# Performance work log

Hardware: AMD Instinct MI355X
Metric: run time of the kernel (lower is better)

Reference implementation:

```python
import jax, jax.numpy as jnp
import numpy as np

N_NODES = 100000
N_EDGES = 1000000
D = 64
N_LAYERS = 3
N_GRAPHS = 64


def _sage_layer(x, src, dst, W_l, b_l, W_r, n_nodes):
    # PyG SAGEConv (aggr='mean'): out = lin_l(mean_{j in N(i)} x_j) + lin_r(x_i)
    msgs = x[src]  # [E, d] gather
    agg = jax.ops.segment_sum(msgs, dst, num_segments=n_nodes)  # [N, d]
    deg = jax.ops.segment_sum(jnp.ones((src.shape[0],), x.dtype), dst, num_segments=n_nodes)
    agg = agg / jnp.maximum(deg, 1.0)[:, None]
    return agg @ W_l + b_l + x @ W_r


def setup_inputs() -> dict:
    key = jax.random.key(0)
    k = jax.random.split(key, 6)
    scale = 1.0 / np.sqrt(D)
    x = jax.random.normal(k[0], (N_NODES, D), dtype=jnp.float32)
    edge_index = jax.random.randint(k[1], (2, N_EDGES), 0, N_NODES, dtype=jnp.int64)
    batch = jnp.sort(jax.random.randint(k[2], (N_NODES,), 0, N_GRAPHS, dtype=jnp.int64))
    Wl = jax.random.normal(k[3], (N_LAYERS, D, D), dtype=jnp.float32) * scale
    bl = jax.random.normal(k[4], (N_LAYERS, D), dtype=jnp.float32) * scale
    Wr = jax.random.normal(k[5], (N_LAYERS, D, D), dtype=jnp.float32) * scale
    return {"x": x, "edge_index": edge_index, "batch": batch,
            "Wl": Wl, "bl": bl, "Wr": Wr, "num_graphs": N_GRAPHS}


def reference(x, edge_index, batch, Wl, bl, Wr, num_graphs):
    src, dst = edge_index[0], edge_index[1]
    n_nodes = x.shape[0]
    for l in range(Wl.shape[0]):  # small fixed number of layers
        x = _sage_layer(x, src, dst, Wl[l], bl[l], Wr[l], n_nodes)
    # per-graph masked mean pooling == segment mean over batch ids
    sums = jax.ops.segment_sum(x, batch, num_segments=num_graphs)  # [G, d]
    counts = jax.ops.segment_sum(jnp.ones((n_nodes,), x.dtype), batch, num_segments=num_graphs)
    return sums / jnp.maximum(counts, 1.0)[:, None]
```

## Files before the change

### kernel.cpp

```cpp
#include <hip/hip_runtime.h>


#define DD 64
#define NBA 128
#define CAP 4096

typedef __attribute__((ext_vector_type(8))) short short8;
typedef __attribute__((ext_vector_type(4))) float f32x4;

__device__ inline short8 pack4(unsigned a, unsigned b, unsigned c, unsigned d) {
    union { uint4 u; short8 s; } un;
    un.u = make_uint4(a, b, c, d);
    return un.s;
}

__device__ inline short8 as_short8(uint4 u) {
    union { uint4 u4; short8 s; } un;
    un.u4 = u;
    return un.s;
}

__device__ inline unsigned rne_bf16(float v) {
    unsigned u = __float_as_uint(v);
    return (u + 0x7FFFu + ((u >> 16) & 1u)) >> 16;
}

__global__ __launch_bounds__(256) void bucket_count(
    const int* __restrict__ dst, int* __restrict__ cnt, int E, int NBUCK) {
    extern __shared__ int hist[];
    const int b = blockIdx.x;
    const int per = (E + NBA - 1) / NBA;
    const int lo = b * per, hi = min(lo + per, E);
    for (int k = threadIdx.x; k < NBUCK; k += 256) hist[k] = 0;
    __syncthreads();
    for (int e = lo + threadIdx.x; e < hi; e += 256)
        atomicAdd(&hist[dst[e] >> 8], 1);
    __syncthreads();
    for (int k = threadIdx.x; k < NBUCK; k += 256)
        cnt[b * NBUCK + k] = hist[k];
}

__global__ __launch_bounds__(256) void bucket_prescan(
    const int* __restrict__ cnt, int* __restrict__ base,
    int* __restrict__ tot, int NBUCK) {
    const int lane = threadIdx.x & 63;
    const int k = (int)((blockIdx.x * 256 + threadIdx.x) >> 6);
    if (k >= NBUCK) return;
    int v0 = cnt[(size_t)lane * NBUCK + k];
    int v1 = cnt[(size_t)(lane + 64) * NBUCK + k];
    int s0 = v0, s1 = v1;
#pragma unroll
    for (int o = 1; o < 64; o <<= 1) {
        const int u0 = __shfl_up(s0, o, 64);
        const int u1 = __shfl_up(s1, o, 64);
        if (lane >= o) { s0 += u0; s1 += u1; }
    }
    const int total0 = __shfl(s0, 63, 64);
    base[(size_t)lane * NBUCK + k] = s0 - v0;
    base[(size_t)(lane + 64) * NBUCK + k] = total0 + s1 - v1;
    if (lane == 63) tot[k] = total0 + s1;
}

__global__ __launch_bounds__(1024) void bucket_toff(
    const int* __restrict__ tot, int* __restrict__ boff,
    int* __restrict__ offs, int NBUCK, int E, int N) {
    __shared__ int s[1024];
    __shared__ int carry_s;
    const int t = threadIdx.x;
    if (t == 0) carry_s = 0;
    __syncthreads();
    for (int cs = 0; cs < NBUCK; cs += 1024) {
        const int i = cs + t;
        const int v = (i < NBUCK) ? tot[i] : 0;
        s[t] = v;
        __syncthreads();
        for (int o = 1; o < 1024; o <<= 1) {
            const int a = (t >= o) ? s[t - o] : 0;
            __syncthreads();
            s[t] += a;
            __syncthreads();
        }
        const int carry = carry_s;
        if (i < NBUCK) boff[i] = carry + s[t] - v;
        __syncthreads();
        if (t == 1023) carry_s = carry + s[1023];
        __syncthreads();
    }
    if (t == 0) { boff[NBUCK] = E; offs[N] = E; }
}

__global__ __launch_bounds__(256) void bucket_scatter(
    const int* __restrict__ src, const int* __restrict__ dst,
    const int* __restrict__ base, const int* __restrict__ boff,
    unsigned* __restrict__ ebuf, int E, int NBUCK) {
    extern __shared__ int pos[];
    const int b = blockIdx.x;
    const int per = (E + NBA - 1) / NBA;
    const int lo = b * per, hi = min(lo + per, E);
    for (int k = threadIdx.x; k < NBUCK; k += 256)
        pos[k] = base[b * NBUCK + k] + boff[k];
    __syncthreads();
    for (int e = lo + threadIdx.x; e < hi; e += 256) {
        const int d = dst[e];
        const int s = src[e];
        const int p = atomicAdd(&pos[d >> 8], 1);
        ebuf[p] = ((unsigned)(d & 255) << 24) | (unsigned)s;
    }
}

__global__ __launch_bounds__(256) void bucket_sort(
    const unsigned* __restrict__ ebuf, const int* __restrict__ boff,
    int* __restrict__ offs, int* __restrict__ adj, int N) {
    const int b  = blockIdx.x;
    const int lo = boff[b];
    const int sz = boff[b + 1] - lo;
    const int base = b << 8;
    const int t = threadIdx.x;

    __shared__ int hist[256];
    __shared__ int hcur[256];
    __shared__ unsigned sbuf[CAP];

    hist[t] = 0;
    __syncthreads();
    for (int i = t; i < sz; i += 256)
        atomicAdd(&hist[ebuf[lo + i] >> 24], 1);
    __syncthreads();
    int v = hist[t];
    hcur[t] = v;
    __syncthreads();
    for (int o = 1; o < 256; o <<= 1) {
        const int a = (t >= o) ? hcur[t - o] : 0;
        __syncthreads();
        hcur[t] += a;
        __syncthreads();
    }
    const int ex = hcur[t] - v;
    __syncthreads();
    hcur[t] = ex;
    if (base + t < N) offs[base + t] = lo + ex;
    __syncthreads();

    if (sz <= CAP) {
        for (int i = t; i < sz; i += 256) {
            const unsigned w = ebuf[lo + i];
            const int p = atomicAdd(&hcur[w >> 24], 1);
            sbuf[p] = w & 0x00FFFFFFu;
        }
        __syncthreads();
        for (int i = t; i < sz; i += 256) adj[lo + i] = (int)sbuf[i];
    } else {
        for (int i = t; i < sz; i += 256) {
            const unsigned w = ebuf[lo + i];
            const int p = atomicAdd(&hcur[w >> 24], 1);
            adj[lo + p] = (int)(w & 0x00FFFFFFu);
        }
    }
}

__global__ __launch_bounds__(256) void cast_bf16(
    const float* __restrict__ in, unsigned short* __restrict__ outb, long long n8) {
    const long long t = (long long)blockIdx.x * 256 + threadIdx.x;
    if (t >= n8) return;
    const float4 v0 = *reinterpret_cast<const float4*>(in + t * 8);
    const float4 v1 = *reinterpret_cast<const float4*>(in + t * 8 + 4);
    uint4 o;
    o.x = rne_bf16(v0.x) | (rne_bf16(v0.y) << 16);
    o.y = rne_bf16(v0.z) | (rne_bf16(v0.w) << 16);
    o.z = rne_bf16(v1.x) | (rne_bf16(v1.y) << 16);
    o.w = rne_bf16(v1.z) | (rne_bf16(v1.w) << 16);
    *reinterpret_cast<uint4*>(outb + t * 8) = o;
}

__global__ __launch_bounds__(256) void aggregate_bf16(
    const unsigned short* __restrict__ xb, float* __restrict__ agg,
    const int* __restrict__ offs, const int* __restrict__ adj, int n) {
    const int t  = blockIdx.x * 256 + threadIdx.x;
    const int nd = t >> 3;
    const int c8 = (t & 7) * 8;
    if (nd >= n) return;

    const int s = offs[nd];
    const int e = offs[nd + 1];

    float a0[8], a1[8], a2[8], a3[8];
#pragma unroll
    for (int p = 0; p < 8; ++p) { a0[p] = 0.f; a1[p] = 0.f; a2[p] = 0.f; a3[p] = 0.f; }

#define ACC8(A, U)                                                             \
    do {                                                                       \
        A[0] += __uint_as_float((U).x << 16);                                  \
        A[1] += __uint_as_float((U).x & 0xFFFF0000u);                          \
        A[2] += __uint_as_float((U).y << 16);                                  \
        A[3] += __uint_as_float((U).y & 0xFFFF0000u);                          \
        A[4] += __uint_as_float((U).z << 16);                                  \
        A[5] += __uint_as_float((U).z & 0xFFFF0000u);                          \
        A[6] += __uint_as_float((U).w << 16);                                  \
        A[7] += __uint_as_float((U).w & 0xFFFF0000u);                          \
    } while (0)

    int j = s;
    for (; j + 4 <= e; j += 4) {
        const int i0 = adj[j], i1 = adj[j + 1], i2 = adj[j + 2], i3 = adj[j + 3];
        const uint4 u0 = *reinterpret_cast<const uint4*>(xb + (size_t)i0 * DD + c8);
        const uint4 u1 = *reinterpret_cast<const uint4*>(xb + (size_t)i1 * DD + c8);
        const uint4 u2 = *reinterpret_cast<const uint4*>(xb + (size_t)i2 * DD + c8);
        const uint4 u3 = *reinterpret_cast<const uint4*>(xb + (size_t)i3 * DD + c8);
        ACC8(a0, u0); ACC8(a1, u1); ACC8(a2, u2); ACC8(a3, u3);
    }
    for (; j < e; ++j) {
        const uint4 u = *reinterpret_cast<const uint4*>(xb + (size_t)adj[j] * DD + c8);
        ACC8(a0, u);
    }
#undef ACC8

    const int deg = e - s;
    const float inv = (deg > 0) ? (1.0f / (float)deg) : 1.0f;
    float4 r0, r1;
    r0.x = (a0[0] + a1[0] + a2[0] + a3[0]) * inv;
    r0.y = (a0[1] + a1[1] + a2[1] + a3[1]) * inv;
    r0.z = (a0[2] + a1[2] + a2[2] + a3[2]) * inv;
    r0.w = (a0[3] + a1[3] + a2[3] + a3[3]) * inv;
    r1.x = (a0[4] + a1[4] + a2[4] + a3[4]) * inv;
    r1.y = (a0[5] + a1[5] + a2[5] + a3[5]) * inv;
    r1.z = (a0[6] + a1[6] + a2[6] + a3[6]) * inv;
    r1.w = (a0[7] + a1[7] + a2[7] + a3[7]) * inv;
    *reinterpret_cast<float4*>(agg + (size_t)nd * DD + c8)     = r0;
    *reinterpret_cast<float4*>(agg + (size_t)nd * DD + c8 + 4) = r1;
}

__global__ void pack_B(const float* __restrict__ Wl, const float* __restrict__ Wr,
                       unsigned* __restrict__ Bp, int L) {
    int t = blockIdx.x * 256 + threadIdx.x;
    int wv = t >> 6, lane = t & 63;
    if (wv >= L * 16) return;
    int layer = wv >> 4;
    int fid = wv & 15;
    int ks = fid >> 2, nt = fid & 3;
    int j = nt * 16 + (lane & 15);
    int kb = ks * 32 + (lane >> 4) * 8;
    const float* wl = Wl + (size_t)layer * DD * DD;
    const float* wr = Wr + (size_t)layer * DD * DD;
    unsigned hi[8], lo[8];
#pragma unroll
    for (int s = 0; s < 8; ++s) {
        int k = kb + s;
        float v = (k < DD) ? wl[k * DD + j] : wr[(k - DD) * DD + j];
        unsigned u = __float_as_uint(v);
        unsigned h = u & 0xFFFF0000u;
        hi[s] = h;
        float lf = v - __uint_as_float(h);
        lo[s] = __float_as_uint(lf) & 0xFFFF0000u;
    }
    size_t base_hi = ((size_t)(layer * 2 + 0) * 16 + fid) * 64 + lane;
    size_t base_lo = ((size_t)(layer * 2 + 1) * 16 + fid) * 64 + lane;
#pragma unroll
    for (int p = 0; p < 4; ++p) {
        Bp[base_hi * 4 + p] = (hi[2 * p] >> 16) | hi[2 * p + 1];
        Bp[base_lo * 4 + p] = (lo[2 * p] >> 16) | lo[2 * p + 1];
    }
}

__global__ __launch_bounds__(256, 2) void mfma_gemm(
    const float* __restrict__ g, const unsigned short* __restrict__ xb,
    unsigned short* __restrict__ outb, const unsigned* __restrict__ Bp,
    const float* __restrict__ bias, int n) {
    const int lane = threadIdx.x & 63;
    const int wv   = (int)((blockIdx.x * 256 + threadIdx.x) >> 6);
    const int nwv  = (int)((gridDim.x * 256) >> 6);

    short8 Bh[4][4], Bl[4][4];
#pragma unroll
    for (int ks = 0; ks < 4; ++ks)
#pragma unroll
        for (int nt = 0; nt < 4; ++nt) {
            int fid = ks * 4 + nt;
            const uint4 h = *reinterpret_cast<const uint4*>(Bp + ((size_t)fid * 64 + lane) * 4);
            const uint4 l = *reinterpret_cast<const uint4*>(Bp + ((size_t)(16 + fid) * 64 + lane) * 4);
            Bh[ks][nt] = pack4(h.x, h.y, h.z, h.w);
            Bl[ks][nt] = pack4(l.x, l.y, l.z, l.w);
        }

    float bv[4];
#pragma unroll
    for (int nt = 0; nt < 4; ++nt) bv[nt] = bias[nt * 16 + (lane & 15)];

    const int ntiles = (n + 15) >> 4;
    for (int tile = wv; tile < ntiles; tile += nwv) {
        const int row = tile * 16 + (lane & 15);
        const bool ok = row < n;
        const float*          grow = g  + (size_t)row * DD + (lane >> 4) * 8;
        const unsigned short* xrow = xb + (size_t)row * DD + (lane >> 4) * 8;

        f32x4 acc[4];
#pragma unroll
        for (int nt = 0; nt < 4; ++nt) acc[nt] = (f32x4){bv[nt], bv[nt], bv[nt], bv[nt]};

#pragma unroll
        for (int ks = 0; ks < 2; ++ks) {
            const float* base = grow + ks * 32;
            f32x4 v0 = ok ? *reinterpret_cast<const f32x4*>(base)
                          : (f32x4){0.f, 0.f, 0.f, 0.f};
            f32x4 v1 = ok ? *reinterpret_cast<const f32x4*>(base + 4)
                          : (f32x4){0.f, 0.f, 0.f, 0.f};
            float vv[8] = {v0[0], v0[1], v0[2], v0[3], v1[0], v1[1], v1[2], v1[3]};
            unsigned hu[4], lu[4];
#pragma unroll
            for (int p = 0; p < 4; ++p) {
                unsigned ua = __float_as_uint(vv[2 * p]);
                unsigned ub = __float_as_uint(vv[2 * p + 1]);
                unsigned ha = ua & 0xFFFF0000u, hb = ub & 0xFFFF0000u;
                hu[p] = (ha >> 16) | hb;
                float la = vv[2 * p]     - __uint_as_float(ha);
                float lb = vv[2 * p + 1] - __uint_as_float(hb);
                lu[p] = ((__float_as_uint(la) & 0xFFFF0000u) >> 16) |
                        (__float_as_uint(lb) & 0xFFFF0000u);
            }
            const short8 Ah = pack4(hu[0], hu[1], hu[2], hu[3]);
            const short8 Al = pack4(lu[0], lu[1], lu[2], lu[3]);
#pragma unroll
            for (int nt = 0; nt < 4; ++nt) {
                acc[nt] = __builtin_amdgcn_mfma_f32_16x16x32_bf16(Ah, Bh[ks][nt], acc[nt], 0, 0, 0);
                acc[nt] = __builtin_amdgcn_mfma_f32_16x16x32_bf16(Al, Bh[ks][nt], acc[nt], 0, 0, 0);
                acc[nt] = __builtin_amdgcn_mfma_f32_16x16x32_bf16(Ah, Bl[ks][nt], acc[nt], 0, 0, 0);
            }
        }

#pragma unroll
        for (int ks = 2; ks < 4; ++ks) {
            const uint4 u = ok ? *reinterpret_cast<const uint4*>(xrow + (ks & 1) * 32)
                               : make_uint4(0, 0, 0, 0);
            const short8 Ah = as_short8(u);
#pragma unroll
            for (int nt = 0; nt < 4; ++nt) {
                acc[nt] = __builtin_amdgcn_mfma_f32_16x16x32_bf16(Ah, Bh[ks][nt], acc[nt], 0, 0, 0);
                acc[nt] = __builtin_amdgcn_mfma_f32_16x16x32_bf16(Ah, Bl[ks][nt], acc[nt], 0, 0, 0);
            }
        }

        const int r0 = tile * 16 + (lane >> 4) * 4;
#pragma unroll
        for (int r = 0; r < 4; ++r) {
            const int rr = r0 + r;
            if (rr < n) {
#pragma unroll
                for (int nt = 0; nt < 4; ++nt) {
                    const size_t idx = (size_t)rr * DD + nt * 16 + (lane & 15);
                    outb[idx] = (unsigned short)rne_bf16(acc[nt][r]);
                }
            }
        }
    }
}

__global__ __launch_bounds__(256) void pool_partial2(
    const float* __restrict__ xa, const unsigned short* __restrict__ xb,
    const int* __restrict__ batch,
    float* __restrict__ sumsA, float* __restrict__ sumsB, int n) {
    const int lane = threadIdx.x & 63;
    const int wv   = (int)((blockIdx.x * blockDim.x + threadIdx.x) >> 6);
    const int nwv  = (int)((gridDim.x * blockDim.x) >> 6);
    const int chunk = (n + nwv - 1) / nwv;
    const int start = wv * chunk;
    if (start >= n) return;
    const int end = min(start + chunk, n);

    int g = batch[start];
    float accA = 0.f, accB = 0.f;
    for (int nd = start; nd < end; ++nd) {
        const int bg = batch[nd];
        if (bg != g) {
            atomicAdd(&sumsA[(size_t)g * DD + lane], accA);
            atomicAdd(&sumsB[(size_t)g * DD + lane], accB);
            accA = 0.f; accB = 0.f;
            g = bg;
        }
        accA += xa[(size_t)nd * DD + lane];
        accB += __uint_as_float((unsigned)xb[(size_t)nd * DD + lane] << 16);
    }
    atomicAdd(&sumsA[(size_t)g * DD + lane], accA);
    atomicAdd(&sumsB[(size_t)g * DD + lane], accB);
}

__global__ void final_gemm(const float* __restrict__ sumsA, const float* __restrict__ sumsX,
                           const int* __restrict__ batch,
                           const float* __restrict__ Wl, const float* __restrict__ bl,
                           const float* __restrict__ Wr,
                           float* __restrict__ out, int n) {
    const int g = blockIdx.x;
    const int d = threadIdx.x;

    int lo = 0, hi = n;
    while (lo < hi) { int m = (lo + hi) >> 1; if (batch[m] < g) lo = m + 1; else hi = m; }
    const int st = lo;
    lo = 0; hi = n;
    while (lo < hi) { int m = (lo + hi) >> 1; if (batch[m] < g + 1) lo = m + 1; else hi = m; }
    const int c = lo - st;

    if (c == 0) {
        out[(size_t)g * DD + d] = 0.f;
        return;
    }
    const float inv = 1.0f / (float)c;

    __shared__ float sa[DD], sx[DD];
    sa[d] = sumsA[(size_t)g * DD + d] * inv;
    sx[d] = sumsX[(size_t)g * DD + d] * inv;
    __syncthreads();

    float acc = bl[d];
#pragma unroll 8
    for (int k = 0; k < DD; ++k) acc += sa[k] * Wl[k * DD + d];
#pragma unroll 8
    for (int k = 0; k < DD; ++k) acc += sx[k] * Wr[k * DD + d];
    out[(size_t)g * DD + d] = acc;
}

extern "C" void kernel_launch(void* const* d_in, const int* in_sizes, int n_in,
                              void* d_out, int out_size, void* d_ws, size_t ws_size,
                              hipStream_t stream) {
    const float* x     = (const float*)d_in[0];
    const int*   ei    = (const int*)d_in[1];
    const int*   batch = (const int*)d_in[2];
    const float* Wl    = (const float*)d_in[3];
    const float* bl    = (const float*)d_in[4];
    const float* Wr    = (const float*)d_in[5];

    const int N = in_sizes[0] / DD;
    const int E = in_sizes[1] / 2;
    const int L = in_sizes[3] / (DD * DD);
    const int G = out_size / DD;
    const int NBUCK = (N + 255) >> 8;

    const int* src = ei;
    const int* dst = ei + E;

    char* ws = (char*)d_ws;
    size_t off = 0;
    auto alloc = [&](size_t bytes) -> char* {
        char* p = ws + off;
        off += (bytes + 255) & ~(size_t)255;
        return p;
    };
    int*      offs   = (int*)alloc((size_t)(N + 1) * 4);
    int*      adj    = (int*)alloc((size_t)E * 4);
    int*      cnt    = (int*)alloc((size_t)NBA * NBUCK * 4);
    int*      basep  = (int*)alloc((size_t)NBA * NBUCK * 4);
    int*      boff   = (int*)alloc((size_t)(NBUCK + 1) * 4);
    int*      tot    = (int*)alloc((size_t)NBUCK * 4);
    unsigned* ebuf   = (unsigned*)alloc((size_t)E * 4);
    float*    aggbuf = (float*)alloc((size_t)N * DD * 4);
    unsigned* Bp     = (unsigned*)alloc((size_t)L * 2 * 16 * 64 * 4 * 4);
    float*    sumsA  = (float*)alloc((size_t)G * DD * 4);
    float*    sumsX  = (float*)alloc((size_t)G * DD * 4);
    const size_t bfbytes = (size_t)N * DD * 2;
    unsigned short* bfIn = (unsigned short*)alloc(bfbytes);
    unsigned short* bf0  = (unsigned short*)alloc(bfbytes);

    const size_t ldsN = (size_t)NBUCK * 4;
    bucket_count<<<NBA, 256, ldsN, stream>>>(dst, cnt, E, NBUCK);
    bucket_prescan<<<(NBUCK * 64 + 255) / 256, 256, 0, stream>>>(cnt, basep, tot, NBUCK);
    bucket_toff<<<1, 1024, 0, stream>>>(tot, boff, offs, NBUCK, E, N);
    bucket_scatter<<<NBA, 256, ldsN, stream>>>(src, dst, basep, boff, ebuf, E, NBUCK);
    bucket_sort<<<NBUCK, 256, 0, stream>>>(ebuf, boff, offs, adj, N);

    pack_B<<<(L * 16 * 64 + 255) / 256, 256, 0, stream>>>(Wl, Wr, Bp, L);

    const long long n8 = (long long)N * DD / 8;
    cast_bf16<<<(int)((n8 + 255) / 256), 256, 0, stream>>>(x, bfIn, n8);

    const unsigned short* curb = bfIn;
    unsigned short* bfs[2] = {bf0, bfIn};
    const int aggB_blocks = (N * 8 + 255) / 256;
    for (int l = 0; l < L - 1; ++l) {
        aggregate_bf16<<<aggB_blocks, 256, 0, stream>>>(curb, aggbuf, offs, adj, N);
        mfma_gemm<<<1024, 256, 0, stream>>>(aggbuf, curb, bfs[l & 1],
                                            Bp + (size_t)l * 2 * 16 * 64 * 4,
                                            bl + (size_t)l * DD, N);
        curb = bfs[l & 1];
    }

    aggregate_bf16<<<aggB_blocks, 256, 0, stream>>>(curb, aggbuf, offs, adj, N);
    hipMemsetAsync(sumsA, 0, (size_t)G * DD * 4, stream);
    hipMemsetAsync(sumsX, 0, (size_t)G * DD * 4, stream);
    pool_partial2<<<2048, 256, 0, stream>>>(aggbuf, curb, batch, sumsA, sumsX, N);
    final_gemm<<<G, DD, 0, stream>>>(sumsA, sumsX, batch,
                                     Wl + (size_t)(L - 1) * DD * DD,
                                     bl + (size_t)(L - 1) * DD,
                                     Wr + (size_t)(L - 1) * DD * DD,
                                     (float*)d_out, N);
}
```

Measured before the change: 185.1 us.

## Store aggregated neighbor means as bf16 and drop split-precision MFMA

The aggregate kernel now rounds its mean output to bf16 instead of writing fp32. The GEMM consumes it directly as a single bf16 operand, dropping the hi/lo split and one third of the MFMAs on the aggregated half, and pooling reads bf16 too. The aggregation loop also gains an 8-wide unroll for more gathers in flight, and the two sumsA/sumsX memsets are merged into one, which relies on the two buffers being adjacent. This halves aggregate-buffer traffic and cuts GEMM work, at the cost of less precision in the aggregated features.

Measured after the change: 178.1 us. 3.8% less time.

```diff
diff --git a/kernel.cpp b/kernel.cpp
--- a/kernel.cpp
+++ b/kernel.cpp
@@ -173,7 +173,7 @@
 }
 
 __global__ __launch_bounds__(256) void aggregate_bf16(
-    const unsigned short* __restrict__ xb, float* __restrict__ agg,
+    const unsigned short* __restrict__ xb, unsigned short* __restrict__ aggb,
     const int* __restrict__ offs, const int* __restrict__ adj, int n) {
     const int t  = blockIdx.x * 256 + threadIdx.x;
     const int nd = t >> 3;
@@ -200,6 +200,20 @@
     } while (0)
 
     int j = s;
+    for (; j + 8 <= e; j += 8) {
+        const int i0 = adj[j],     i1 = adj[j + 1], i2 = adj[j + 2], i3 = adj[j + 3];
+        const int i4 = adj[j + 4], i5 = adj[j + 5], i6 = adj[j + 6], i7 = adj[j + 7];
+        const uint4 u0 = *reinterpret_cast<const uint4*>(xb + (size_t)i0 * DD + c8);
+        const uint4 u1 = *reinterpret_cast<const uint4*>(xb + (size_t)i1 * DD + c8);
+        const uint4 u2 = *reinterpret_cast<const uint4*>(xb + (size_t)i2 * DD + c8);
+        const uint4 u3 = *reinterpret_cast<const uint4*>(xb + (size_t)i3 * DD + c8);
+        const uint4 u4 = *reinterpret_cast<const uint4*>(xb + (size_t)i4 * DD + c8);
+        const uint4 u5 = *reinterpret_cast<const uint4*>(xb + (size_t)i5 * DD + c8);
+        const uint4 u6 = *reinterpret_cast<const uint4*>(xb + (size_t)i6 * DD + c8);
+        const uint4 u7 = *reinterpret_cast<const uint4*>(xb + (size_t)i7 * DD + c8);
+        ACC8(a0, u0); ACC8(a1, u1); ACC8(a2, u2); ACC8(a3, u3);
+        ACC8(a0, u4); ACC8(a1, u5); ACC8(a2, u6); ACC8(a3, u7);
+    }
     for (; j + 4 <= e; j += 4) {
         const int i0 = adj[j], i1 = adj[j + 1], i2 = adj[j + 2], i3 = adj[j + 3];
         const uint4 u0 = *reinterpret_cast<const uint4*>(xb + (size_t)i0 * DD + c8);
@@ -216,17 +230,15 @@
 
     const int deg = e - s;
     const float inv = (deg > 0) ? (1.0f / (float)deg) : 1.0f;
-    float4 r0, r1;
-    r0.x = (a0[0] + a1[0] + a2[0] + a3[0]) * inv;
-    r0.y = (a0[1] + a1[1] + a2[1] + a3[1]) * inv;
-    r0.z = (a0[2] + a1[2] + a2[2] + a3[2]) * inv;
-    r0.w = (a0[3] + a1[3] + a2[3] + a3[3]) * inv;
-    r1.x = (a0[4] + a1[4] + a2[4] + a3[4]) * inv;
-    r1.y = (a0[5] + a1[5] + a2[5] + a3[5]) * inv;
-    r1.z = (a0[6] + a1[6] + a2[6] + a3[6]) * inv;
-    r1.w = (a0[7] + a1[7] + a2[7] + a3[7]) * inv;
-    *reinterpret_cast<float4*>(agg + (size_t)nd * DD + c8)     = r0;
-    *reinterpret_cast<float4*>(agg + (size_t)nd * DD + c8 + 4) = r1;
+    float r[8];
+#pragma unroll
+    for (int p = 0; p < 8; ++p) r[p] = (a0[p] + a1[p] + a2[p] + a3[p]) * inv;
+    uint4 o;
+    o.x = rne_bf16(r[0]) | (rne_bf16(r[1]) << 16);
+    o.y = rne_bf16(r[2]) | (rne_bf16(r[3]) << 16);
+    o.z = rne_bf16(r[4]) | (rne_bf16(r[5]) << 16);
+    o.w = rne_bf16(r[6]) | (rne_bf16(r[7]) << 16);
+    *reinterpret_cast<uint4*>(aggb + (size_t)nd * DD + c8) = o;
 }
 
 __global__ void pack_B(const float* __restrict__ Wl, const float* __restrict__ Wr,
@@ -262,7 +274,7 @@
 }
 
 __global__ __launch_bounds__(256, 2) void mfma_gemm(
-    const float* __restrict__ g, const unsigned short* __restrict__ xb,
+    const unsigned short* __restrict__ gb, const unsigned short* __restrict__ xb,
     unsigned short* __restrict__ outb, const unsigned* __restrict__ Bp,
     const float* __restrict__ bias, int n) {
     const int lane = threadIdx.x & 63;
@@ -289,7 +301,7 @@
     for (int tile = wv; tile < ntiles; tile += nwv) {
         const int row = tile * 16 + (lane & 15);
         const bool ok = row < n;
-        const float*          grow = g  + (size_t)row * DD + (lane >> 4) * 8;
+        const unsigned short* grow = gb + (size_t)row * DD + (lane >> 4) * 8;
         const unsigned short* xrow = xb + (size_t)row * DD + (lane >> 4) * 8;
 
         f32x4 acc[4];
@@ -297,38 +309,9 @@
         for (int nt = 0; nt < 4; ++nt) acc[nt] = (f32x4){bv[nt], bv[nt], bv[nt], bv[nt]};
 
 #pragma unroll
-        for (int ks = 0; ks < 2; ++ks) {
-            const float* base = grow + ks * 32;
-            f32x4 v0 = ok ? *reinterpret_cast<const f32x4*>(base)
-                          : (f32x4){0.f, 0.f, 0.f, 0.f};
-            f32x4 v1 = ok ? *reinterpret_cast<const f32x4*>(base + 4)
-                          : (f32x4){0.f, 0.f, 0.f, 0.f};
-            float vv[8] = {v0[0], v0[1], v0[2], v0[3], v1[0], v1[1], v1[2], v1[3]};
-            unsigned hu[4], lu[4];
-#pragma unroll
-            for (int p = 0; p < 4; ++p) {
-                unsigned ua = __float_as_uint(vv[2 * p]);
-                unsigned ub = __float_as_uint(vv[2 * p + 1]);
-                unsigned ha = ua & 0xFFFF0000u, hb = ub & 0xFFFF0000u;
-                hu[p] = (ha >> 16) | hb;
-                float la = vv[2 * p]     - __uint_as_float(ha);
-                float lb = vv[2 * p + 1] - __uint_as_float(hb);
-                lu[p] = ((__float_as_uint(la) & 0xFFFF0000u) >> 16) |
-                        (__float_as_uint(lb) & 0xFFFF0000u);
-            }
-            const short8 Ah = pack4(hu[0], hu[1], hu[2], hu[3]);
-            const short8 Al = pack4(lu[0], lu[1], lu[2], lu[3]);
-#pragma unroll
-            for (int nt = 0; nt < 4; ++nt) {
-                acc[nt] = __builtin_amdgcn_mfma_f32_16x16x32_bf16(Ah, Bh[ks][nt], acc[nt], 0, 0, 0);
-                acc[nt] = __builtin_amdgcn_mfma_f32_16x16x32_bf16(Al, Bh[ks][nt], acc[nt], 0, 0, 0);
-                acc[nt] = __builtin_amdgcn_mfma_f32_16x16x32_bf16(Ah, Bl[ks][nt], acc[nt], 0, 0, 0);
-            }
-        }
-
-#pragma unroll
-        for (int ks = 2; ks < 4; ++ks) {
-            const uint4 u = ok ? *reinterpret_cast<const uint4*>(xrow + (ks & 1) * 32)
+        for (int ks = 0; ks < 4; ++ks) {
+            const unsigned short* base = ((ks < 2) ? grow : xrow) + (ks & 1) * 32;
+            const uint4 u = ok ? *reinterpret_cast<const uint4*>(base)
                                : make_uint4(0, 0, 0, 0);
             const short8 Ah = as_short8(u);
 #pragma unroll
@@ -354,7 +337,7 @@
 }
 
 __global__ __launch_bounds__(256) void pool_partial2(
-    const float* __restrict__ xa, const unsigned short* __restrict__ xb,
+    const unsigned short* __restrict__ xa, const unsigned short* __restrict__ xb,
     const int* __restrict__ batch,
     float* __restrict__ sumsA, float* __restrict__ sumsB, int n) {
     const int lane = threadIdx.x & 63;
@@ -375,7 +358,7 @@
             accA = 0.f; accB = 0.f;
             g = bg;
         }
-        accA += xa[(size_t)nd * DD + lane];
+        accA += __uint_as_float((unsigned)xa[(size_t)nd * DD + lane] << 16);
         accB += __uint_as_float((unsigned)xb[(size_t)nd * DD + lane] << 16);
     }
     atomicAdd(&sumsA[(size_t)g * DD + lane], accA);
@@ -449,11 +432,11 @@
     int*      boff   = (int*)alloc((size_t)(NBUCK + 1) * 4);
     int*      tot    = (int*)alloc((size_t)NBUCK * 4);
     unsigned* ebuf   = (unsigned*)alloc((size_t)E * 4);
-    float*    aggbuf = (float*)alloc((size_t)N * DD * 4);
+    const size_t bfbytes = (size_t)N * DD * 2;
+    unsigned short* aggb = (unsigned short*)alloc(bfbytes);
     unsigned* Bp     = (unsigned*)alloc((size_t)L * 2 * 16 * 64 * 4 * 4);
     float*    sumsA  = (float*)alloc((size_t)G * DD * 4);
     float*    sumsX  = (float*)alloc((size_t)G * DD * 4);
-    const size_t bfbytes = (size_t)N * DD * 2;
     unsigned short* bfIn = (unsigned short*)alloc(bfbytes);
     unsigned short* bf0  = (unsigned short*)alloc(bfbytes);
 
@@ -473,17 +456,16 @@
     unsigned short* bfs[2] = {bf0, bfIn};
     const int aggB_blocks = (N * 8 + 255) / 256;
     for (int l = 0; l < L - 1; ++l) {
-        aggregate_bf16<<<aggB_blocks, 256, 0, stream>>>(curb, aggbuf, offs, adj, N);
-        mfma_gemm<<<1024, 256, 0, stream>>>(aggbuf, curb, bfs[l & 1],
+        aggregate_bf16<<<aggB_blocks, 256, 0, stream>>>(curb, aggb, offs, adj, N);
+        mfma_gemm<<<1024, 256, 0, stream>>>(aggb, curb, bfs[l & 1],
                                             Bp + (size_t)l * 2 * 16 * 64 * 4,
                                             bl + (size_t)l * DD, N);
         curb = bfs[l & 1];
     }
 
-    aggregate_bf16<<<aggB_blocks, 256, 0, stream>>>(curb, aggbuf, offs, adj, N);
-    hipMemsetAsync(sumsA, 0, (size_t)G * DD * 4, stream);
-    hipMemsetAsync(sumsX, 0, (size_t)G * DD * 4, stream);
-    pool_partial2<<<2048, 256, 0, stream>>>(aggbuf, curb, batch, sumsA, sumsX, N);
+    aggregate_bf16<<<aggB_blocks, 256, 0, stream>>>(curb, aggb, offs, adj, N);
+    hipMemsetAsync(sumsA, 0, (size_t)G * DD * 4 * 2, stream);
+    pool_partial2<<<2048, 256, 0, stream>>>(aggb, curb, batch, sumsA, sumsX, N);
     final_gemm<<<G, DD, 0, stream>>>(sumsA, sumsX, batch,
                                      Wl + (size_t)(L - 1) * DD * DD,
                                      bl + (size_t)(L - 1) * DD,
```
